# Kernel tuning notes

Hardware: AMD Instinct MI355X
Metric: run time of the kernel (lower is better)

## Reference

```python
import jax, jax.numpy as jnp
import numpy as np

B, S, D = 8, 4096, 512
BLOCK, LEFT, RIGHT = 64, 1, 1
FF = 2048
EPS = 1e-6


def setup_inputs() -> dict:
    key = jax.random.key(0)
    ks = jax.random.split(key, 16)
    sd = 1.0 / np.sqrt(D)
    sf = 1.0 / np.sqrt(FF)
    return {
        "x": jax.random.normal(ks[0], (B, S, D), jnp.float32),
        "Wq": jax.random.normal(ks[1], (D, D), jnp.float32) * sd,
        "bq": jnp.zeros((D,), jnp.float32),
        "Wk": jax.random.normal(ks[2], (D, D), jnp.float32) * sd,
        "bk": jnp.zeros((D,), jnp.float32),
        "Wv": jax.random.normal(ks[3], (D, D), jnp.float32) * sd,
        "bv": jnp.zeros((D,), jnp.float32),
        "W1": jax.random.normal(ks[4], (D, FF), jnp.float32) * sd,
        "b1": jnp.zeros((FF,), jnp.float32),
        "W2": jax.random.normal(ks[5], (FF, D), jnp.float32) * sf,
        "b2": jnp.zeros((D,), jnp.float32),
        "g1": jnp.ones((D,), jnp.float32),
        "be1": jnp.zeros((D,), jnp.float32),
        "g2": jnp.ones((D,), jnp.float32),
        "be2": jnp.zeros((D,), jnp.float32),
    }


def layernorm(x, g, b):
    m = jnp.mean(x, axis=-1, keepdims=True)
    v = jnp.mean(jnp.square(x - m), axis=-1, keepdims=True)
    return g * (x - m) * jax.lax.rsqrt(v + EPS) + b


def local_attention(x, Wq, bq, Wk, bk, Wv, bv):
    Bsz, Sl, Dm = x.shape
    nb = Sl // BLOCK          # number of blocks
    nw = LEFT + RIGHT + 1     # window (in blocks)
    q = (x @ Wq + bq).reshape(Bsz, nb, BLOCK, Dm)
    k = (x @ Wk + bk).reshape(Bsz, nb, BLOCK, Dm)
    v = (x @ Wv + bv).reshape(Bsz, nb, BLOCK, Dm)
    # pad block axis so every query block has LEFT/RIGHT neighbor blocks
    kp = jnp.pad(k, ((0, 0), (LEFT, RIGHT), (0, 0), (0, 0)))
    vp = jnp.pad(v, ((0, 0), (LEFT, RIGHT), (0, 0), (0, 0)))
    # gather windows: (B, nb, nw*BLOCK, D)
    k_win = jnp.stack([kp[:, j:j + nb] for j in range(nw)], axis=2).reshape(Bsz, nb, nw * BLOCK, Dm)
    v_win = jnp.stack([vp[:, j:j + nb] for j in range(nw)], axis=2).reshape(Bsz, nb, nw * BLOCK, Dm)
    # mask out-of-range (padded) blocks at sequence edges
    blk = jnp.arange(nb)[:, None] + jnp.arange(nw)[None, :] - LEFT  # (nb, nw)
    mask = ((blk >= 0) & (blk < nb))
    mask = jnp.repeat(mask, BLOCK, axis=1)  # (nb, nw*BLOCK)
    scores = jnp.einsum('bnqd,bnkd->bnqk', q, k_win) / jnp.sqrt(jnp.float32(Dm))
    scores = jnp.where(mask[None, :, None, :], scores, jnp.float32(-1e9))
    attn = jax.nn.softmax(scores, axis=-1)
    out = jnp.einsum('bnqk,bnkd->bnqd', attn, v_win)
    return out.reshape(Bsz, Sl, Dm)


def reference(x, Wq, bq, Wk, bk, Wv, bv, W1, b1, W2, b2, g1, be1, g2, be2):
    # inference mode: dropout is identity
    a = local_attention(x, Wq, bq, Wk, bk, Wv, bv)
    out1 = layernorm(x + a, g1, be1)
    ffn = jnp.maximum(out1 @ W1 + b1, 0.0) @ W2 + b2
    return layernorm(out1 + ffn, g2, be2)
```

## Files before the change

### kernel.cpp

```cpp
#include <hip/hip_runtime.h>


typedef __bf16 bf16;
typedef __bf16 bf16x8 __attribute__((ext_vector_type(8)));
typedef float  f32x4  __attribute__((ext_vector_type(4)));

#define DEV __device__ __forceinline__

#define BAR()  do { asm volatile("" ::: "memory"); __builtin_amdgcn_s_barrier(); asm volatile("" ::: "memory"); } while (0)
#define WAITV0() asm volatile("s_waitcnt vmcnt(0)" ::: "memory")
#define WAITL()  asm volatile("s_waitcnt lgkmcnt(0)" ::: "memory")

DEV void gload_lds16(const void* g, void* lds) {
  __builtin_amdgcn_global_load_lds(
      (const __attribute__((address_space(1))) void*)g,
      (__attribute__((address_space(3))) void*)lds, 16, 0, 0);
}

__global__ __launch_bounds__(256) void cast_to_bf16(const float* __restrict__ in,
                                                    bf16* __restrict__ out, int n8) {
  int i = blockIdx.x * 256 + threadIdx.x;
  if (i >= n8) return;
  float4 a0 = ((const float4*)in)[i * 2];
  float4 a1 = ((const float4*)in)[i * 2 + 1];
  bf16x8 o;
  o[0] = (bf16)a0.x; o[1] = (bf16)a0.y; o[2] = (bf16)a0.z; o[3] = (bf16)a0.w;
  o[4] = (bf16)a1.x; o[5] = (bf16)a1.y; o[6] = (bf16)a1.z; o[7] = (bf16)a1.w;
  ((bf16x8*)out)[i] = o;
}

__global__ __launch_bounds__(256) void transpose_cast(const float* __restrict__ W,
                                                      bf16* __restrict__ Wt, int K, int N) {
  __shared__ bf16 tile[64][66];
  const int n0 = blockIdx.x * 64, k0 = blockIdx.y * 64;
  const int t = threadIdx.x;
#pragma unroll
  for (int it = 0; it < 16; ++it) {
    int c = it * 256 + t;
    int kr = c >> 6, nc = c & 63;
    tile[nc][kr] = (bf16)W[(size_t)(k0 + kr) * N + n0 + nc];
  }
  __syncthreads();
#pragma unroll
  for (int it = 0; it < 2; ++it) {
    int c = it * 256 + t;
    int nr = c >> 3, kg = (c & 7) * 8;
    bf16x8 v;
#pragma unroll
    for (int e = 0; e < 8; ++e) v[e] = tile[nr][kg + e];
    *(bf16x8*)(Wt + (size_t)(n0 + nr) * K + k0 + kg) = v;
  }
}

__global__ __launch_bounds__(256) void concat_bias(const float* __restrict__ bq,
                                                   const float* __restrict__ bk,
                                                   const float* __restrict__ bv,
                                                   float* __restrict__ o) {
  int i = blockIdx.x * 256 + threadIdx.x;
  if (i < 512) o[i] = bq[i];
  else if (i < 1024) o[i] = bk[i - 512];
  else if (i < 1536) o[i] = bv[i - 1024];
}

template <int RELU, int F32OUT>
__global__ __launch_bounds__(512, 1)
void gemm256(const bf16* __restrict__ A, const bf16* __restrict__ Bt,
             const float* __restrict__ bias, void* __restrict__ Cout,
             int M, int N, int K) {
  __shared__ bf16x8 lds8[8192];
  char* const LB = (char*)lds8;
  const int tid = threadIdx.x;
  const int w = tid >> 6, l = tid & 63;
  const int lr = l & 15, lg = l >> 4;
  const int wm = w >> 2, wn = w & 3;

  const int nwg = gridDim.x * gridDim.y;
  const int bid = blockIdx.y * gridDim.x + blockIdx.x;
  const int cpx = nwg >> 3;
  const int swzb = (bid & 7) * cpx + (bid >> 3);
  const int m0 = (swzb & 127) * 256;
  const int n0 = (swzb >> 7) * 256;

  const int NT = K >> 6;

  const int srow = tid >> 3;
  const int scol = (((tid & 7) ^ (srow & 7)) << 3);

  const int swz0 = ((lg ^ (lr & 7)) << 4);
  const int swz1 = (((4 + lg) ^ (lr & 7)) << 4);

  f32x4 acc[8][4];
#pragma unroll
  for (int i = 0; i < 8; ++i)
#pragma unroll
    for (int j = 0; j < 4; ++j) acc[i][j] = f32x4{0.f, 0.f, 0.f, 0.f};

  auto stage = [&](int ht) {
    const int th = ht >> 2;
    const int h = ht & 1;
    const bf16* g = ((ht & 2) ? (Bt + (size_t)(n0 + h * 128 + srow) * K)
                              : (A + (size_t)(m0 + h * 128 + srow) * K))
                    + th * 64 + scol;
    char* d = LB + (((th & 1) << 16) | ((ht & 3) << 14)) + tid * 16;
    gload_lds16(g, d);
    gload_lds16(g + (size_t)64 * K, d + 8192);
  };

#pragma unroll
  for (int p = 0; p < 4; ++p) stage(p);
  WAITV0();
  BAR();

  for (int t = 0; t < NT; ++t) {
    const char* pA = LB + ((t & 1) << 16) + (wm << 14) + lr * 128;
    const char* pB = LB + ((t & 1) << 16) + 32768 + ((wn >> 1) << 14) +
                     (((wn & 1) << 6) + lr) * 128;
    bf16x8 bq[4][2];
#pragma unroll
    for (int q = 0; q < 4; ++q) {
      bf16x8 a0k0 = *(const bf16x8*)(pA + (2 * q) * 2048 + swz0);
      bf16x8 a0k1 = *(const bf16x8*)(pA + (2 * q) * 2048 + swz1);
      bf16x8 a1k0 = *(const bf16x8*)(pA + (2 * q + 1) * 2048 + swz0);
      bf16x8 a1k1 = *(const bf16x8*)(pA + (2 * q + 1) * 2048 + swz1);
      if (q == 0) {
#pragma unroll
        for (int n = 0; n < 4; ++n) {
          bq[n][0] = *(const bf16x8*)(pB + n * 2048 + swz0);
          bq[n][1] = *(const bf16x8*)(pB + n * 2048 + swz1);
        }
      }
      if (q < 2 && t + 1 < NT) {
        stage(4 * (t + 1) + 2 * q);
        stage(4 * (t + 1) + 2 * q + 1);
      }
      BAR();
      WAITL();
      __builtin_amdgcn_s_setprio(1);
#pragma unroll
      for (int n = 0; n < 4; ++n) {
        acc[2 * q][n]     = __builtin_amdgcn_mfma_f32_16x16x32_bf16(a0k0, bq[n][0], acc[2 * q][n], 0, 0, 0);
        acc[2 * q + 1][n] = __builtin_amdgcn_mfma_f32_16x16x32_bf16(a1k0, bq[n][0], acc[2 * q + 1][n], 0, 0, 0);
      }
#pragma unroll
      for (int n = 0; n < 4; ++n) {
        acc[2 * q][n]     = __builtin_amdgcn_mfma_f32_16x16x32_bf16(a0k1, bq[n][1], acc[2 * q][n], 0, 0, 0);
        acc[2 * q + 1][n] = __builtin_amdgcn_mfma_f32_16x16x32_bf16(a1k1, bq[n][1], acc[2 * q + 1][n], 0, 0, 0);
      }
      __builtin_amdgcn_s_setprio(0);
      if (q == 3 && t + 1 < NT) WAITV0();
      BAR();
    }
  }

  if (!F32OUT) {
    bf16* cl = (bf16*)LB;
#pragma unroll
    for (int n = 0; n < 4; ++n) {
      const int col = (wn << 6) + (n << 4) + lr;
      const float bv = bias[n0 + col];
#pragma unroll
      for (int m = 0; m < 8; ++m)
#pragma unroll
        for (int rg = 0; rg < 4; ++rg) {
          const int row = (wm << 7) + (m << 4) + (lg << 2) + rg;
          float v = acc[m][n][rg] + bv;
          if (RELU) v = fmaxf(v, 0.f);
          cl[row * 256 + col] = (bf16)v;
        }
    }
    WAITL();
    BAR();
    bf16* Cb = (bf16*)Cout;
#pragma unroll
    for (int it = 0; it < 16; ++it) {
      const int idx = it * 512 + tid;
      const int r = idx >> 5, ch = idx & 31;
      *(bf16x8*)(Cb + (size_t)(m0 + r) * N + n0 + (ch << 3)) =
          *(const bf16x8*)(cl + r * 256 + (ch << 3));
    }
  } else {
    float* Cf = (float*)Cout;
#pragma unroll
    for (int n = 0; n < 4; ++n) {
      const int col = n0 + (wn << 6) + (n << 4) + lr;
      const float bv = bias[col];
#pragma unroll
      for (int m = 0; m < 8; ++m)
#pragma unroll
        for (int rg = 0; rg < 4; ++rg) {
          const int row = m0 + (wm << 7) + (m << 4) + (lg << 2) + rg;
          float v = acc[m][n][rg] + bv;
          if (RELU) v = fmaxf(v, 0.f);
          Cf[(size_t)row * N + col] = v;
        }
    }
  }
}

__global__ __launch_bounds__(256) void transpose_v(const bf16* __restrict__ qkv,
                                                   bf16* __restrict__ vt) {
  __shared__ bf16 tile[64][66];
  const int s0 = blockIdx.x * 64, d0 = blockIdx.y * 64, b = blockIdx.z;
  const int t = threadIdx.x;
#pragma unroll
  for (int it = 0; it < 2; ++it) {
    int c = it * 256 + t;
    int r = c >> 3, g = (c & 7) * 8;
    bf16x8 v = *(const bf16x8*)(qkv + ((size_t)b * 4096 + s0 + r) * 1536 + 1024 + d0 + g);
#pragma unroll
    for (int e = 0; e < 8; ++e) tile[g + e][r] = v[e];
  }
  __syncthreads();
#pragma unroll
  for (int it = 0; it < 2; ++it) {
    int c = it * 256 + t;
    int dr = c >> 3, sg = (c & 7) * 8;
    bf16x8 v;
#pragma unroll
    for (int e = 0; e < 8; ++e) v[e] = tile[dr][sg + e];
    *(bf16x8*)(vt + ((size_t)b * 512 + d0 + dr) * 4096 + s0 + sg) = v;
  }
}

__global__ __launch_bounds__(256, 2)
void attn_local(const bf16* __restrict__ qkv, const bf16* __restrict__ vt,
                bf16* __restrict__ aout) {
  __shared__ bf16 P[4][16][200];
  const int qb = blockIdx.x, b = blockIdx.y;
  const int t = threadIdx.x, w = t >> 6, l = t & 63;
  const int lr = l & 15, lg = l >> 4;
  const int jlo = (qb == 0) ? 1 : 0;
  const int jhi = (qb == 63) ? 2 : 3;
  const size_t qrow = (size_t)b * 4096 + qb * 64 + w * 16;
  const bf16* qp = qkv + (qrow + lr) * 1536 + lg * 8;

  f32x4 S[3][4];
#pragma unroll
  for (int j = 0; j < 3; ++j)
#pragma unroll
    for (int n = 0; n < 4; ++n) S[j][n] = f32x4{0.f, 0.f, 0.f, 0.f};

  for (int kk = 0; kk < 16; ++kk) {
    bf16x8 aq = *(const bf16x8*)(qp + kk * 32);
#pragma unroll
    for (int j = 0; j < 3; ++j) {
      if (j < jlo || j >= jhi) continue;
      const bf16* kp = qkv + ((size_t)b * 4096 + (qb - 1 + j) * 64) * 1536 + 512;
#pragma unroll
      for (int n = 0; n < 4; ++n) {
        bf16x8 bk = *(const bf16x8*)(kp + (size_t)(n * 16 + lr) * 1536 + kk * 32 + lg * 8);
        S[j][n] = __builtin_amdgcn_mfma_f32_16x16x32_bf16(aq, bk, S[j][n], 0, 0, 0);
      }
    }
  }

  const float scale = 0.044194173824159216f;
  float mx[4] = {-3e38f, -3e38f, -3e38f, -3e38f};
#pragma unroll
  for (int j = 0; j < 3; ++j) {
    if (j < jlo || j >= jhi) continue;
#pragma unroll
    for (int n = 0; n < 4; ++n)
#pragma unroll
      for (int i = 0; i < 4; ++i) mx[i] = fmaxf(mx[i], S[j][n][i]);
  }
#pragma unroll
  for (int i = 0; i < 4; ++i) {
    mx[i] = fmaxf(mx[i], __shfl_xor(mx[i], 1));
    mx[i] = fmaxf(mx[i], __shfl_xor(mx[i], 2));
    mx[i] = fmaxf(mx[i], __shfl_xor(mx[i], 4));
    mx[i] = fmaxf(mx[i], __shfl_xor(mx[i], 8));
  }
  float sm[4] = {0.f, 0.f, 0.f, 0.f};
#pragma unroll
  for (int j = 0; j < 3; ++j) {
    if (j < jlo || j >= jhi) continue;
#pragma unroll
    for (int n = 0; n < 4; ++n)
#pragma unroll
      for (int i = 0; i < 4; ++i) {
        float p = __expf((S[j][n][i] - mx[i]) * scale);
        S[j][n][i] = p;
        sm[i] += p;
      }
  }
#pragma unroll
  for (int i = 0; i < 4; ++i) {
    sm[i] += __shfl_xor(sm[i], 1);
    sm[i] += __shfl_xor(sm[i], 2);
    sm[i] += __shfl_xor(sm[i], 4);
    sm[i] += __shfl_xor(sm[i], 8);
  }
#pragma unroll
  for (int j = 0; j < 3; ++j) {
    if (j < jlo || j >= jhi) continue;
#pragma unroll
    for (int n = 0; n < 4; ++n)
#pragma unroll
      for (int i = 0; i < 4; ++i)
        P[w][lg * 4 + i][j * 64 + n * 16 + lr] = (bf16)S[j][n][i];
  }
  float rinv[4];
#pragma unroll
  for (int i = 0; i < 4; ++i) rinv[i] = 1.f / sm[i];

  const bf16* vtb = vt + (size_t)b * 512 * 4096;
  const long scol = (long)qb * 64 - 64;

#pragma unroll
  for (int ch = 0; ch < 4; ++ch) {
    f32x4 O[8];
#pragma unroll
    for (int n = 0; n < 8; ++n) O[n] = f32x4{0.f, 0.f, 0.f, 0.f};
#pragma unroll
    for (int j = 0; j < 3; ++j) {
      if (j < jlo || j >= jhi) continue;
#pragma unroll
      for (int k2 = 0; k2 < 2; ++k2) {
        bf16x8 ap = *(const bf16x8*)&P[w][lr][j * 64 + k2 * 32 + lg * 8];
#pragma unroll
        for (int n = 0; n < 8; ++n) {
          const bf16* vp = vtb + (long)(ch * 128 + n * 16 + lr) * 4096 +
                           (scol + j * 64 + k2 * 32 + lg * 8);
          bf16x8 bv = *(const bf16x8*)vp;
          O[n] = __builtin_amdgcn_mfma_f32_16x16x32_bf16(ap, bv, O[n], 0, 0, 0);
        }
      }
    }
#pragma unroll
    for (int n = 0; n < 8; ++n)
#pragma unroll
      for (int rg = 0; rg < 4; ++rg) {
        size_t row = qrow + lg * 4 + rg;
        aout[row * 512 + ch * 128 + n * 16 + lr] = (bf16)(O[n][rg] * rinv[rg]);
      }
  }
}

__global__ __launch_bounds__(256) void ln_res1(const float* __restrict__ x,
                                               const bf16* __restrict__ a,
                                               const float* __restrict__ g,
                                               const float* __restrict__ be,
                                               bf16* __restrict__ out) {
  const int t = threadIdx.x, w = t >> 6, l = t & 63;
  const size_t row = (size_t)blockIdx.x * 4 + w;
  const float* xp = x + row * 512 + l * 8;
  float4 x0 = ((const float4*)xp)[0];
  float4 x1 = ((const float4*)xp)[1];
  bf16x8 av = *(const bf16x8*)(a + row * 512 + l * 8);
  float s[8] = {x0.x + (float)av[0], x0.y + (float)av[1], x0.z + (float)av[2], x0.w + (float)av[3],
                x1.x + (float)av[4], x1.y + (float)av[5], x1.z + (float)av[6], x1.w + (float)av[7]};
  float sum = 0.f;
#pragma unroll
  for (int i = 0; i < 8; ++i) sum += s[i];
#pragma unroll
  for (int m = 1; m <= 32; m <<= 1) sum += __shfl_xor(sum, m);
  const float mean = sum * (1.f / 512.f);
  float vs = 0.f;
#pragma unroll
  for (int i = 0; i < 8; ++i) { float d = s[i] - mean; vs += d * d; }
#pragma unroll
  for (int m = 1; m <= 32; m <<= 1) vs += __shfl_xor(vs, m);
  const float r = rsqrtf(vs * (1.f / 512.f) + 1e-6f);
  float4 g0 = ((const float4*)(g + l * 8))[0], g1 = ((const float4*)(g + l * 8))[1];
  float4 b0 = ((const float4*)(be + l * 8))[0], b1 = ((const float4*)(be + l * 8))[1];
  bf16x8 o;
  o[0] = (bf16)(g0.x * (s[0] - mean) * r + b0.x);
  o[1] = (bf16)(g0.y * (s[1] - mean) * r + b0.y);
  o[2] = (bf16)(g0.z * (s[2] - mean) * r + b0.z);
  o[3] = (bf16)(g0.w * (s[3] - mean) * r + b0.w);
  o[4] = (bf16)(g1.x * (s[4] - mean) * r + b1.x);
  o[5] = (bf16)(g1.y * (s[5] - mean) * r + b1.y);
  o[6] = (bf16)(g1.z * (s[6] - mean) * r + b1.z);
  o[7] = (bf16)(g1.w * (s[7] - mean) * r + b1.w);
  *(bf16x8*)(out + row * 512 + l * 8) = o;
}

__global__ __launch_bounds__(256) void ln_res2(const bf16* __restrict__ o1,
                                               float* __restrict__ y,
                                               const float* __restrict__ g,
                                               const float* __restrict__ be) {
  const int t = threadIdx.x, w = t >> 6, l = t & 63;
  const size_t row = (size_t)blockIdx.x * 4 + w;
  float* yp = y + row * 512 + l * 8;
  float4 y0 = ((const float4*)yp)[0];
  float4 y1 = ((const float4*)yp)[1];
  bf16x8 ov = *(const bf16x8*)(o1 + row * 512 + l * 8);
  float s[8] = {y0.x + (float)ov[0], y0.y + (float)ov[1], y0.z + (float)ov[2], y0.w + (float)ov[3],
                y1.x + (float)ov[4], y1.y + (float)ov[5], y1.z + (float)ov[6], y1.w + (float)ov[7]};
  float sum = 0.f;
#pragma unroll
  for (int i = 0; i < 8; ++i) sum += s[i];
#pragma unroll
  for (int m = 1; m <= 32; m <<= 1) sum += __shfl_xor(sum, m);
  const float mean = sum * (1.f / 512.f);
  float vs = 0.f;
#pragma unroll
  for (int i = 0; i < 8; ++i) { float d = s[i] - mean; vs += d * d; }
#pragma unroll
  for (int m = 1; m <= 32; m <<= 1) vs += __shfl_xor(vs, m);
  const float r = rsqrtf(vs * (1.f / 512.f) + 1e-6f);
  float4 g0 = ((const float4*)(g + l * 8))[0], g1 = ((const float4*)(g + l * 8))[1];
  float4 b0 = ((const float4*)(be + l * 8))[0], b1 = ((const float4*)(be + l * 8))[1];
  float4 r0, r1;
  r0.x = g0.x * (s[0] - mean) * r + b0.x;
  r0.y = g0.y * (s[1] - mean) * r + b0.y;
  r0.z = g0.z * (s[2] - mean) * r + b0.z;
  r0.w = g0.w * (s[3] - mean) * r + b0.w;
  r1.x = g1.x * (s[4] - mean) * r + b1.x;
  r1.y = g1.y * (s[5] - mean) * r + b1.y;
  r1.z = g1.z * (s[6] - mean) * r + b1.z;
  r1.w = g1.w * (s[7] - mean) * r + b1.w;
  ((float4*)yp)[0] = r0;
  ((float4*)yp)[1] = r1;
}

extern "C" void kernel_launch(void* const* d_in, const int* in_sizes, int n_in,
                              void* d_out, int out_size, void* d_ws, size_t ws_size,
                              hipStream_t stream) {
  const float* x   = (const float*)d_in[0];
  const float* Wq  = (const float*)d_in[1];
  const float* bq  = (const float*)d_in[2];
  const float* Wk  = (const float*)d_in[3];
  const float* bk  = (const float*)d_in[4];
  const float* Wv  = (const float*)d_in[5];
  const float* bv  = (const float*)d_in[6];
  const float* W1  = (const float*)d_in[7];
  const float* b1  = (const float*)d_in[8];
  const float* W2  = (const float*)d_in[9];
  const float* b2  = (const float*)d_in[10];
  const float* g1  = (const float*)d_in[11];
  const float* be1 = (const float*)d_in[12];
  const float* g2  = (const float*)d_in[13];
  const float* be2 = (const float*)d_in[14];
  float* out = (float*)d_out;

  char* ws = (char*)d_ws;
  bf16*  WqkvT = (bf16*)(ws + 0);
  bf16*  W1T   = (bf16*)(ws + 1572864);
  bf16*  W2T   = (bf16*)(ws + 3670016);
  float* bqkv  = (float*)(ws + 5767168);
  bf16*  xb    = (bf16*)(ws + 6291456);
  bf16*  out1  = (bf16*)(ws + 39845888);
  bf16*  qkv   = (bf16*)(ws + 73400320);
  bf16*  vtb   = (bf16*)(ws + 174063616);
  bf16*  a_    = xb;
  bf16*  h     = qkv;

  cast_to_bf16<<<8192, 256, 0, stream>>>(x, xb, 2097152);
  transpose_cast<<<dim3(8, 8), 256, 0, stream>>>(Wq, WqkvT, 512, 512);
  transpose_cast<<<dim3(8, 8), 256, 0, stream>>>(Wk, WqkvT + 262144, 512, 512);
  transpose_cast<<<dim3(8, 8), 256, 0, stream>>>(Wv, WqkvT + 524288, 512, 512);
  transpose_cast<<<dim3(32, 8), 256, 0, stream>>>(W1, W1T, 512, 2048);
  transpose_cast<<<dim3(8, 32), 256, 0, stream>>>(W2, W2T, 2048, 512);
  concat_bias<<<6, 256, 0, stream>>>(bq, bk, bv, bqkv);

  gemm256<0, 0><<<dim3(128, 6), 512, 0, stream>>>(xb, WqkvT, bqkv, qkv, 32768, 1536, 512);
  transpose_v<<<dim3(64, 8, 8), 256, 0, stream>>>(qkv, vtb);
  attn_local<<<dim3(64, 8), 256, 0, stream>>>(qkv, vtb, a_);
  ln_res1<<<8192, 256, 0, stream>>>(x, a_, g1, be1, out1);
  gemm256<1, 0><<<dim3(128, 8), 512, 0, stream>>>(out1, W1T, b1, h, 32768, 2048, 512);
  gemm256<0, 1><<<dim3(128, 2), 512, 0, stream>>>(h, W2T, b2, out, 32768, 512, 2048);
  ln_res2<<<8192, 256, 0, stream>>>(out1, out, g2, be2);
}
```

Measured before the change: 429.9 us.

## Triple-buffer GEMM with K=32 tiles and split attention across more workgroups

The GEMM mainloop now uses 32-wide K tiles in a three-stage LDS ring buffer (96KB instead of 128KB). A and B loads are issued two iterations ahead and interleaved with the two halves of the MFMA work, with partial vmcnt waits. The bf16 epilogue writes out one half-tile at a time to fit the smaller LDS. Separately, attn_local launches four times as many workgroups: each handles 16 query rows, with each wave covering a 128-column slice of the output instead of looping over four chunks, and occupancy hints are raised. This trades redundant QK/softmax computation per workgroup for more parallelism and lower register pressure.

Measured after the change: 651.7 us. 51.6% more time.

```diff
diff --git a/kernel.cpp b/kernel.cpp
--- a/kernel.cpp
+++ b/kernel.cpp
@@ -8,7 +8,7 @@
 #define DEV __device__ __forceinline__
 
 #define BAR()  do { asm volatile("" ::: "memory"); __builtin_amdgcn_s_barrier(); asm volatile("" ::: "memory"); } while (0)
-#define WAITV0() asm volatile("s_waitcnt vmcnt(0)" ::: "memory")
+#define WAITV(n) asm volatile("s_waitcnt vmcnt(" #n ")" ::: "memory")
 #define WAITL()  asm volatile("s_waitcnt lgkmcnt(0)" ::: "memory")
 
 DEV void gload_lds16(const void* g, void* lds) {
@@ -67,7 +67,7 @@
 void gemm256(const bf16* __restrict__ A, const bf16* __restrict__ Bt,
              const float* __restrict__ bias, void* __restrict__ Cout,
              int M, int N, int K) {
-  __shared__ bf16x8 lds8[8192];
+  __shared__ bf16x8 lds8[6144];
   char* const LB = (char*)lds8;
   const int tid = threadIdx.x;
   const int w = tid >> 6, l = tid & 63;
@@ -81,13 +81,12 @@
   const int m0 = (swzb & 127) * 256;
   const int n0 = (swzb >> 7) * 256;
 
-  const int NT = K >> 6;
-
-  const int srow = tid >> 3;
-  const int scol = (((tid & 7) ^ (srow & 7)) << 3);
-
-  const int swz0 = ((lg ^ (lr & 7)) << 4);
-  const int swz1 = (((4 + lg) ^ (lr & 7)) << 4);
+  const int NT = K >> 5;
+
+  const int srow = tid >> 2;
+  const int scol = (((tid & 3) ^ (srow & 3)) << 3);
+
+  const int swz = ((lg ^ (lr & 3)) << 4);
 
   f32x4 acc[8][4];
 #pragma unroll
@@ -95,88 +94,119 @@
 #pragma unroll
     for (int j = 0; j < 4; ++j) acc[i][j] = f32x4{0.f, 0.f, 0.f, 0.f};
 
-  auto stage = [&](int ht) {
-    const int th = ht >> 2;
-    const int h = ht & 1;
-    const bf16* g = ((ht & 2) ? (Bt + (size_t)(n0 + h * 128 + srow) * K)
-                              : (A + (size_t)(m0 + h * 128 + srow) * K))
-                    + th * 64 + scol;
-    char* d = LB + (((th & 1) << 16) | ((ht & 3) << 14)) + tid * 16;
+  auto stageA = [&](int t) {
+    const bf16* g = A + (size_t)(m0 + srow) * K + t * 32 + scol;
+    char* d = LB + (t % 3) * 32768 + tid * 16;
     gload_lds16(g, d);
-    gload_lds16(g + (size_t)64 * K, d + 8192);
+    gload_lds16(g + (size_t)128 * K, d + 8192);
   };
-
-#pragma unroll
-  for (int p = 0; p < 4; ++p) stage(p);
-  WAITV0();
+  auto stageB = [&](int t) {
+    const bf16* g = Bt + (size_t)(n0 + srow) * K + t * 32 + scol;
+    char* d = LB + (t % 3) * 32768 + 16384 + tid * 16;
+    gload_lds16(g, d);
+    gload_lds16(g + (size_t)128 * K, d + 8192);
+  };
+
+  stageA(0); stageB(0);
+  stageA(1); stageB(1);
+  WAITV(4);
   BAR();
 
   for (int t = 0; t < NT; ++t) {
-    const char* pA = LB + ((t & 1) << 16) + (wm << 14) + lr * 128;
-    const char* pB = LB + ((t & 1) << 16) + 32768 + ((wn >> 1) << 14) +
-                     (((wn & 1) << 6) + lr) * 128;
-    bf16x8 bq[4][2];
-#pragma unroll
-    for (int q = 0; q < 4; ++q) {
-      bf16x8 a0k0 = *(const bf16x8*)(pA + (2 * q) * 2048 + swz0);
-      bf16x8 a0k1 = *(const bf16x8*)(pA + (2 * q) * 2048 + swz1);
-      bf16x8 a1k0 = *(const bf16x8*)(pA + (2 * q + 1) * 2048 + swz0);
-      bf16x8 a1k1 = *(const bf16x8*)(pA + (2 * q + 1) * 2048 + swz1);
-      if (q == 0) {
+    const char* base = LB + (t % 3) * 32768;
+    const char* pA = base + (wm << 13) + lr * 64 + swz;
+    const char* pB = base + 16384 + (wn << 12) + lr * 64 + swz;
+    bf16x8 a0, a1, a2, a3, b0, b1, b2, b3;
+    a0 = *(const bf16x8*)(pA);
+    a1 = *(const bf16x8*)(pA + 1024);
+    a2 = *(const bf16x8*)(pA + 2048);
+    a3 = *(const bf16x8*)(pA + 3072);
+    b0 = *(const bf16x8*)(pB);
+    b1 = *(const bf16x8*)(pB + 1024);
+    b2 = *(const bf16x8*)(pB + 2048);
+    b3 = *(const bf16x8*)(pB + 3072);
+    if (t + 2 < NT) stageA(t + 2);
+    BAR();
+    WAITL();
+    __builtin_amdgcn_s_setprio(1);
+    acc[0][0] = __builtin_amdgcn_mfma_f32_16x16x32_bf16(a0, b0, acc[0][0], 0, 0, 0);
+    acc[0][1] = __builtin_amdgcn_mfma_f32_16x16x32_bf16(a0, b1, acc[0][1], 0, 0, 0);
+    acc[0][2] = __builtin_amdgcn_mfma_f32_16x16x32_bf16(a0, b2, acc[0][2], 0, 0, 0);
+    acc[0][3] = __builtin_amdgcn_mfma_f32_16x16x32_bf16(a0, b3, acc[0][3], 0, 0, 0);
+    acc[1][0] = __builtin_amdgcn_mfma_f32_16x16x32_bf16(a1, b0, acc[1][0], 0, 0, 0);
+    acc[1][1] = __builtin_amdgcn_mfma_f32_16x16x32_bf16(a1, b1, acc[1][1], 0, 0, 0);
+    acc[1][2] = __builtin_amdgcn_mfma_f32_16x16x32_bf16(a1, b2, acc[1][2], 0, 0, 0);
+    acc[1][3] = __builtin_amdgcn_mfma_f32_16x16x32_bf16(a1, b3, acc[1][3], 0, 0, 0);
+    acc[2][0] = __builtin_amdgcn_mfma_f32_16x16x32_bf16(a2, b0, acc[2][0], 0, 0, 0);
+    acc[2][1] = __builtin_amdgcn_mfma_f32_16x16x32_bf16(a2, b1, acc[2][1], 0, 0, 0);
+    acc[2][2] = __builtin_amdgcn_mfma_f32_16x16x32_bf16(a2, b2, acc[2][2], 0, 0, 0);
+    acc[2][3] = __builtin_amdgcn_mfma_f32_16x16x32_bf16(a2, b3, acc[2][3], 0, 0, 0);
+    acc[3][0] = __builtin_amdgcn_mfma_f32_16x16x32_bf16(a3, b0, acc[3][0], 0, 0, 0);
+    acc[3][1] = __builtin_amdgcn_mfma_f32_16x16x32_bf16(a3, b1, acc[3][1], 0, 0, 0);
+    acc[3][2] = __builtin_amdgcn_mfma_f32_16x16x32_bf16(a3, b2, acc[3][2], 0, 0, 0);
+    acc[3][3] = __builtin_amdgcn_mfma_f32_16x16x32_bf16(a3, b3, acc[3][3], 0, 0, 0);
+    __builtin_amdgcn_s_setprio(0);
+    BAR();
+    a0 = *(const bf16x8*)(pA + 4096);
+    a1 = *(const bf16x8*)(pA + 5120);
+    a2 = *(const bf16x8*)(pA + 6144);
+    a3 = *(const bf16x8*)(pA + 7168);
+    if (t + 2 < NT) stageB(t + 2);
+    BAR();
+    WAITL();
+    __builtin_amdgcn_s_setprio(1);
+    acc[4][0] = __builtin_amdgcn_mfma_f32_16x16x32_bf16(a0, b0, acc[4][0], 0, 0, 0);
+    acc[4][1] = __builtin_amdgcn_mfma_f32_16x16x32_bf16(a0, b1, acc[4][1], 0, 0, 0);
+    acc[4][2] = __builtin_amdgcn_mfma_f32_16x16x32_bf16(a0, b2, acc[4][2], 0, 0, 0);
+    acc[4][3] = __builtin_amdgcn_mfma_f32_16x16x32_bf16(a0, b3, acc[4][3], 0, 0, 0);
+    acc[5][0] = __builtin_amdgcn_mfma_f32_16x16x32_bf16(a1, b0, acc[5][0], 0, 0, 0);
+    acc[5][1] = __builtin_amdgcn_mfma_f32_16x16x32_bf16(a1, b1, acc[5][1], 0, 0, 0);
+    acc[5][2] = __builtin_amdgcn_mfma_f32_16x16x32_bf16(a1, b2, acc[5][2], 0, 0, 0);
+    acc[5][3] = __builtin_amdgcn_mfma_f32_16x16x32_bf16(a1, b3, acc[5][3], 0, 0, 0);
+    acc[6][0] = __builtin_amdgcn_mfma_f32_16x16x32_bf16(a2, b0, acc[6][0], 0, 0, 0);
+    acc[6][1] = __builtin_amdgcn_mfma_f32_16x16x32_bf16(a2, b1, acc[6][1], 0, 0, 0);
+    acc[6][2] = __builtin_amdgcn_mfma_f32_16x16x32_bf16(a2, b2, acc[6][2], 0, 0, 0);
+    acc[6][3] = __builtin_amdgcn_mfma_f32_16x16x32_bf16(a2, b3, acc[6][3], 0, 0, 0);
+    acc[7][0] = __builtin_amdgcn_mfma_f32_16x16x32_bf16(a3, b0, acc[7][0], 0, 0, 0);
+    acc[7][1] = __builtin_amdgcn_mfma_f32_16x16x32_bf16(a3, b1, acc[7][1], 0, 0, 0);
+    acc[7][2] = __builtin_amdgcn_mfma_f32_16x16x32_bf16(a3, b2, acc[7][2], 0, 0, 0);
+    acc[7][3] = __builtin_amdgcn_mfma_f32_16x16x32_bf16(a3, b3, acc[7][3], 0, 0, 0);
+    __builtin_amdgcn_s_setprio(0);
+    if (t + 2 < NT) { WAITV(4); }
+    else if (t + 2 == NT) { WAITV(0); }
+    BAR();
+  }
+
+  if (!F32OUT) {
+    bf16* cl = (bf16*)LB;
+    bf16* Cb = (bf16*)Cout;
+#pragma unroll
+    for (int half = 0; half < 2; ++half) {
+      if (wm == half) {
 #pragma unroll
         for (int n = 0; n < 4; ++n) {
-          bq[n][0] = *(const bf16x8*)(pB + n * 2048 + swz0);
-          bq[n][1] = *(const bf16x8*)(pB + n * 2048 + swz1);
+          const int col = (wn << 6) + (n << 4) + lr;
+          const float bv = bias[n0 + col];
+#pragma unroll
+          for (int m = 0; m < 8; ++m)
+#pragma unroll
+            for (int rg = 0; rg < 4; ++rg) {
+              const int row = (m << 4) + (lg << 2) + rg;
+              float v = acc[m][n][rg] + bv;
+              if (RELU) v = fmaxf(v, 0.f);
+              cl[row * 256 + col] = (bf16)v;
+            }
         }
       }
-      if (q < 2 && t + 1 < NT) {
-        stage(4 * (t + 1) + 2 * q);
-        stage(4 * (t + 1) + 2 * q + 1);
+      __syncthreads();
+#pragma unroll
+      for (int it = 0; it < 8; ++it) {
+        const int idx = it * 512 + tid;
+        const int r = idx >> 5, ch = idx & 31;
+        *(bf16x8*)(Cb + (size_t)(m0 + half * 128 + r) * N + n0 + (ch << 3)) =
+            *(const bf16x8*)(cl + r * 256 + (ch << 3));
       }
-      BAR();
-      WAITL();
-      __builtin_amdgcn_s_setprio(1);
-#pragma unroll
-      for (int n = 0; n < 4; ++n) {
-        acc[2 * q][n]     = __builtin_amdgcn_mfma_f32_16x16x32_bf16(a0k0, bq[n][0], acc[2 * q][n], 0, 0, 0);
-        acc[2 * q + 1][n] = __builtin_amdgcn_mfma_f32_16x16x32_bf16(a1k0, bq[n][0], acc[2 * q + 1][n], 0, 0, 0);
-      }
-#pragma unroll
-      for (int n = 0; n < 4; ++n) {
-        acc[2 * q][n]     = __builtin_amdgcn_mfma_f32_16x16x32_bf16(a0k1, bq[n][1], acc[2 * q][n], 0, 0, 0);
-        acc[2 * q + 1][n] = __builtin_amdgcn_mfma_f32_16x16x32_bf16(a1k1, bq[n][1], acc[2 * q + 1][n], 0, 0, 0);
-      }
-      __builtin_amdgcn_s_setprio(0);
-      if (q == 3 && t + 1 < NT) WAITV0();
-      BAR();
-    }
-  }
-
-  if (!F32OUT) {
-    bf16* cl = (bf16*)LB;
-#pragma unroll
-    for (int n = 0; n < 4; ++n) {
-      const int col = (wn << 6) + (n << 4) + lr;
-      const float bv = bias[n0 + col];
-#pragma unroll
-      for (int m = 0; m < 8; ++m)
-#pragma unroll
-        for (int rg = 0; rg < 4; ++rg) {
-          const int row = (wm << 7) + (m << 4) + (lg << 2) + rg;
-          float v = acc[m][n][rg] + bv;
-          if (RELU) v = fmaxf(v, 0.f);
-          cl[row * 256 + col] = (bf16)v;
-        }
-    }
-    WAITL();
-    BAR();
-    bf16* Cb = (bf16*)Cout;
-#pragma unroll
-    for (int it = 0; it < 16; ++it) {
-      const int idx = it * 512 + tid;
-      const int r = idx >> 5, ch = idx & 31;
-      *(bf16x8*)(Cb + (size_t)(m0 + r) * N + n0 + (ch << 3)) =
-          *(const bf16x8*)(cl + r * 256 + (ch << 3));
+      __syncthreads();
     }
   } else {
     float* Cf = (float*)Cout;
@@ -222,16 +252,16 @@
   }
 }
 
-__global__ __launch_bounds__(256, 2)
+__global__ __launch_bounds__(256, 6)
 void attn_local(const bf16* __restrict__ qkv, const bf16* __restrict__ vt,
                 bf16* __restrict__ aout) {
   __shared__ bf16 P[4][16][200];
-  const int qb = blockIdx.x, b = blockIdx.y;
+  const int qb = blockIdx.x >> 2, sub = blockIdx.x & 3, b = blockIdx.y;
   const int t = threadIdx.x, w = t >> 6, l = t & 63;
   const int lr = l & 15, lg = l >> 4;
   const int jlo = (qb == 0) ? 1 : 0;
   const int jhi = (qb == 63) ? 2 : 3;
-  const size_t qrow = (size_t)b * 4096 + qb * 64 + w * 16;
+  const size_t qrow = (size_t)b * 4096 + qb * 64 + sub * 16;
   const bf16* qp = qkv + (qrow + lr) * 1536 + lg * 8;
 
   f32x4 S[3][4];
@@ -307,34 +337,31 @@
   const bf16* vtb = vt + (size_t)b * 512 * 4096;
   const long scol = (long)qb * 64 - 64;
 
-#pragma unroll
-  for (int ch = 0; ch < 4; ++ch) {
-    f32x4 O[8];
-#pragma unroll
-    for (int n = 0; n < 8; ++n) O[n] = f32x4{0.f, 0.f, 0.f, 0.f};
-#pragma unroll
-    for (int j = 0; j < 3; ++j) {
-      if (j < jlo || j >= jhi) continue;
-#pragma unroll
-      for (int k2 = 0; k2 < 2; ++k2) {
-        bf16x8 ap = *(const bf16x8*)&P[w][lr][j * 64 + k2 * 32 + lg * 8];
-#pragma unroll
-        for (int n = 0; n < 8; ++n) {
-          const bf16* vp = vtb + (long)(ch * 128 + n * 16 + lr) * 4096 +
-                           (scol + j * 64 + k2 * 32 + lg * 8);
-          bf16x8 bv = *(const bf16x8*)vp;
-          O[n] = __builtin_amdgcn_mfma_f32_16x16x32_bf16(ap, bv, O[n], 0, 0, 0);
-        }
+  f32x4 O[8];
+#pragma unroll
+  for (int n = 0; n < 8; ++n) O[n] = f32x4{0.f, 0.f, 0.f, 0.f};
+#pragma unroll
+  for (int j = 0; j < 3; ++j) {
+    if (j < jlo || j >= jhi) continue;
+#pragma unroll
+    for (int k2 = 0; k2 < 2; ++k2) {
+      bf16x8 ap = *(const bf16x8*)&P[w][lr][j * 64 + k2 * 32 + lg * 8];
+#pragma unroll
+      for (int n = 0; n < 8; ++n) {
+        const bf16* vp = vtb + (long)(w * 128 + n * 16 + lr) * 4096 +
+                         (scol + j * 64 + k2 * 32 + lg * 8);
+        bf16x8 bv = *(const bf16x8*)vp;
+        O[n] = __builtin_amdgcn_mfma_f32_16x16x32_bf16(ap, bv, O[n], 0, 0, 0);
       }
     }
-#pragma unroll
-    for (int n = 0; n < 8; ++n)
-#pragma unroll
-      for (int rg = 0; rg < 4; ++rg) {
-        size_t row = qrow + lg * 4 + rg;
-        aout[row * 512 + ch * 128 + n * 16 + lr] = (bf16)(O[n][rg] * rinv[rg]);
-      }
-  }
+  }
+#pragma unroll
+  for (int n = 0; n < 8; ++n)
+#pragma unroll
+    for (int rg = 0; rg < 4; ++rg) {
+      size_t row = qrow + lg * 4 + rg;
+      aout[row * 512 + w * 128 + n * 16 + lr] = (bf16)(O[n][rg] * rinv[rg]);
+    }
 }
 
 __global__ __launch_bounds__(256) void ln_res1(const float* __restrict__ x,
@@ -457,7 +484,7 @@
 
   gemm256<0, 0><<<dim3(128, 6), 512, 0, stream>>>(xb, WqkvT, bqkv, qkv, 32768, 1536, 512);
   transpose_v<<<dim3(64, 8, 8), 256, 0, stream>>>(qkv, vtb);
-  attn_local<<<dim3(64, 8), 256, 0, stream>>>(qkv, vtb, a_);
+  attn_local<<<dim3(256, 8), 256, 0, stream>>>(qkv, vtb, a_);
   ln_res1<<<8192, 256, 0, stream>>>(x, a_, g1, be1, out1);
   gemm256<1, 0><<<dim3(128, 8), 512, 0, stream>>>(out1, W1T, b1, h, 32768, 2048, 512);
   gemm256<0, 1><<<dim3(128, 2), 512, 0, stream>>>(h, W2T, b2, out, 32768, 512, 2048);
```
